# Kernel optimization log

Hardware: AMD Instinct MI355X
Metric: run time of the kernel (lower is better)

## Reference

```python
import jax, jax.numpy as jnp
import numpy as np
from jax import lax

DIM = 180; NH = 6; WH = 16; WW = 16; MH = 8; MW = 8
HD = DIM // (2 * NH)  # 15, head dim; also the (non-sqrt) scale
RMS_EPS = 1.1920929e-07  # torch.finfo(float32).eps (RMSNorm eps=None)

def _conv(x, w, b, pad):
    # x: NHWC, w: HWIO
    return lax.conv_general_dilated(x, w, (1, 1), [(pad, pad), (pad, pad)],
                                    dimension_numbers=('NHWC', 'HWIO', 'NHWC')) + b

def _lrelu(x):
    return jnp.where(x >= 0, x, 0.2 * x)

def _ln(x, w, b, eps=1e-5):
    m = x.mean(-1, keepdims=True)
    v = jnp.mean((x - m) ** 2, -1, keepdims=True)
    return (x - m) / jnp.sqrt(v + eps) * w + b

def _forward(x, dfe_w1, dfe_b1, dfe_w2, dfe_b2, dfe_w3, dfe_b3, dfe_lw, dfe_lb,
             sl_w, sl_b, pos_pw, pos_pb, ln1w, ln1b, l1w, l1b, ln2w, ln2b,
             l2w, l2b, ln3w, ln3b, l3w, l3b, proj_w, proj_b, norm_w):
    B, C, H, W = x.shape
    xh = jnp.transpose(x, (0, 2, 3, 1))  # NHWC
    shortcut = xh
    # DFE: conv branch gated by 1x1 linear branch
    h = _lrelu(_conv(xh, dfe_w1, dfe_b1, 0))
    h = _lrelu(_conv(h, dfe_w2, dfe_b2, 1))
    h = _conv(h, dfe_w3, dfe_b3, 0)
    qv = h * _conv(xh, dfe_lw, dfe_lb, 0)  # (B,H,W,C)
    # window partition
    L = WH * WW
    qv = qv.reshape(B, H // WH, WH, W // WW, WW, C).transpose(0, 1, 3, 2, 4, 5).reshape(-1, L, C)
    Bw = qv.shape[0]
    qv = qv.reshape(Bw, L, 2, NH, HD).transpose(2, 0, 3, 1, 4)
    q, v = qv[0], qv[1]  # (Bw, NH, L, HD)
    # spatial linear projection of v: downsample window -> base window
    rH, rW = WH // MH, WW // MW
    vp = v.reshape(Bw, NH, MH, rH, MW, rW, HD).transpose(0, 1, 2, 4, 6, 3, 5)
    vp = vp.reshape(Bw, NH, MH * MW, HD, rH * rW)
    vp = ((vp @ sl_w) + sl_b)[..., 0]  # (Bw, NH, mapL, HD)
    corr = jnp.einsum('bhlc,bhmc->bhlm', q, vp) / HD  # (Bw, NH, L, mapL)
    # dynamic relative position bias
    bh = jnp.arange(1 - WH, WH, dtype=jnp.float32)
    bw = jnp.arange(1 - WW, WW, dtype=jnp.float32)
    biases = jnp.stack(jnp.meshgrid(bh, bw, indexing='ij')).reshape(2, -1).T  # (nb, 2)
    p = biases @ pos_pw + pos_pb
    p = jax.nn.relu(_ln(p, ln1w, ln1b)) @ l1w + l1b
    p = jax.nn.relu(_ln(p, ln2w, ln2b)) @ l2w + l2b
    pos = jax.nn.relu(_ln(p, ln3w, ln3b)) @ l3w + l3b  # (nb, NH)
    coords = jnp.stack(jnp.meshgrid(jnp.arange(WH), jnp.arange(WW), indexing='ij')).reshape(2, -1)
    rel = coords[:, :, None] - coords[:, None, :]  # (2, L, L)
    idx = (rel[0] + WH - 1) * (2 * WW - 1) + (rel[1] + WW - 1)  # (L, L)
    rpb = pos[idx.reshape(-1)].reshape(L, MH, rH, MW, rW, NH)
    rpb = rpb.transpose(0, 1, 3, 5, 2, 4).reshape(L, MH * MW, NH, rH * rW).mean(-1)
    rpb = rpb.transpose(2, 0, 1)  # (NH, L, mapL)
    corr = corr + rpb[None]
    xs = jnp.einsum('bhlm,bhmc->bhlc', corr, vp).transpose(0, 2, 1, 3).reshape(Bw, L, NH * HD)
    # channel self-correlation
    qc = q.transpose(0, 2, 1, 3).reshape(Bw, L, NH * HD)
    vc = v.transpose(0, 2, 1, 3).reshape(Bw, L, NH * HD)
    cmap = jnp.einsum('blc,bld->bcd', qc, vc) / L  # (Bw, C/2, C/2)
    xc = jnp.einsum('bcd,bld->blc', cmap, vc)  # (Bw, L, C/2)
    # window reverse
    def wrev(win):
        c = win.shape[-1]
        return win.reshape(B, H // WH, W // WW, WH, WW, c).transpose(0, 1, 3, 2, 4, 5).reshape(B, H, W, c)
    xs = wrev(xs.reshape(Bw, WH, WW, NH * HD))
    xc = wrev(xc.reshape(Bw, WH, WW, NH * HD))
    y = jnp.concatenate([xs, xc], -1)  # (B, H, W, C)
    y = y @ proj_w + proj_b
    y = y * (1.0 / jnp.sqrt(jnp.mean(y * y, -1, keepdims=True) + RMS_EPS)) * norm_w
    y = shortcut + y
    return jnp.transpose(y, (0, 3, 1, 2))


def setup_inputs() -> dict:
    key = jax.random.key(0)
    ks = iter(jax.random.split(key, 32))
    def rn(shape, s=0.05):
        return jax.random.normal(next(ks), shape, jnp.float32) * s
    inp = {}
    inp['x'] = jax.random.normal(next(ks), (4, 180, 256, 256), jnp.float32)
    inp['dfe_w1'] = rn((1, 1, 180, 36)); inp['dfe_b1'] = rn((36,))
    inp['dfe_w2'] = rn((3, 3, 36, 36)); inp['dfe_b2'] = rn((36,))
    inp['dfe_w3'] = rn((1, 1, 36, 180)); inp['dfe_b3'] = rn((180,))
    inp['dfe_lw'] = rn((1, 1, 180, 180)); inp['dfe_lb'] = rn((180,))
    inp['sl_w'] = rn((4, 1)); inp['sl_b'] = rn((1,))
    inp['pos_pw'] = rn((2, 11)); inp['pos_pb'] = rn((11,))
    inp['ln1w'] = jnp.ones((11,)); inp['ln1b'] = jnp.zeros((11,))
    inp['l1w'] = rn((11, 11)); inp['l1b'] = rn((11,))
    inp['ln2w'] = jnp.ones((11,)); inp['ln2b'] = jnp.zeros((11,))
    inp['l2w'] = rn((11, 11)); inp['l2b'] = rn((11,))
    inp['ln3w'] = jnp.ones((11,)); inp['ln3b'] = jnp.zeros((11,))
    inp['l3w'] = rn((11, 6)); inp['l3b'] = rn((6,))
    inp['proj_w'] = rn((180, 180)); inp['proj_b'] = rn((180,))
    inp['norm_w'] = jnp.ones((180,))
    return inp


def reference(x, dfe_w1, dfe_b1, dfe_w2, dfe_b2, dfe_w3, dfe_b3, dfe_lw, dfe_lb,
              sl_w, sl_b, pos_pw, pos_pb, ln1w, ln1b, l1w, l1b, ln2w, ln2b,
              l2w, l2b, ln3w, ln3b, l3w, l3b, proj_w, proj_b, norm_w):
    return _forward(x, dfe_w1, dfe_b1, dfe_w2, dfe_b2, dfe_w3, dfe_b3, dfe_lw, dfe_lb,
                    sl_w, sl_b, pos_pw, pos_pb, ln1w, ln1b, l1w, l1b, ln2w, ln2b,
                    l2w, l2b, ln3w, ln3b, l3w, l3b, proj_w, proj_b, norm_w)
```

## Files before the change

### kernel.cpp

```cpp
#include <hip/hip_runtime.h>
#include <stdint.h>

typedef unsigned short u16;
typedef unsigned int   u32;

#define HW 65536

typedef __bf16 bf16x8 __attribute__((ext_vector_type(8)));
typedef float  f32x4  __attribute__((ext_vector_type(4)));

static __device__ __forceinline__ float bf2f(u16 h) {
    u32 u = ((u32)h) << 16;
    return __builtin_bit_cast(float, u);
}
static __device__ __forceinline__ u16 f2bf(float f) {
    u32 u = __builtin_bit_cast(u32, f);
    u += 0x7fffu + ((u >> 16) & 1u);
    return (u16)(u >> 16);
}
static __device__ __forceinline__ void bf2x2(u32 u, float& a, float& b) {
    a = __builtin_bit_cast(float, u << 16);
    b = __builtin_bit_cast(float, u & 0xffff0000u);
}
static __device__ __forceinline__ f32x4 mfma16(bf16x8 a, bf16x8 b, f32x4 c) {
    return __builtin_amdgcn_mfma_f32_16x16x32_bf16(a, b, c, 0, 0, 0);
}

static __device__ __forceinline__ void lnrelu11(float* p, const float* __restrict__ w,
                                                const float* __restrict__ b) {
    float m = 0.f;
    #pragma unroll
    for (int k = 0; k < 11; k++) m += p[k];
    m *= (1.0f / 11.0f);
    float v = 0.f;
    #pragma unroll
    for (int k = 0; k < 11; k++) { float d = p[k] - m; v = fmaf(d, d, v); }
    v *= (1.0f / 11.0f);
    float r = 1.0f / sqrtf(v + 1e-5f);
    #pragma unroll
    for (int k = 0; k < 11; k++) {
        float t = (p[k] - m) * r * w[k] + b[k];
        p[k] = t > 0.f ? t : 0.f;
    }
}

__global__ __launch_bounds__(1024) void k_pos(
    const float* __restrict__ pw, const float* __restrict__ pb,
    const float* __restrict__ ln1w, const float* __restrict__ ln1b,
    const float* __restrict__ l1w, const float* __restrict__ l1b,
    const float* __restrict__ ln2w, const float* __restrict__ ln2b,
    const float* __restrict__ l2w, const float* __restrict__ l2b,
    const float* __restrict__ ln3w, const float* __restrict__ ln3b,
    const float* __restrict__ l3w, const float* __restrict__ l3b,
    float* __restrict__ pos)
{
    int i = threadIdx.x;
    if (i >= 961) return;
    float b0 = (float)(i / 31) - 15.0f;
    float b1 = (float)(i % 31) - 15.0f;
    float p[11], t[11];
    #pragma unroll
    for (int j = 0; j < 11; j++) p[j] = b0 * pw[j] + b1 * pw[11 + j] + pb[j];
    lnrelu11(p, ln1w, ln1b);
    #pragma unroll
    for (int j = 0; j < 11; j++) {
        float s = l1b[j];
        #pragma unroll
        for (int k = 0; k < 11; k++) s = fmaf(p[k], l1w[k * 11 + j], s);
        t[j] = s;
    }
    lnrelu11(t, ln2w, ln2b);
    #pragma unroll
    for (int j = 0; j < 11; j++) {
        float s = l2b[j];
        #pragma unroll
        for (int k = 0; k < 11; k++) s = fmaf(t[k], l2w[k * 11 + j], s);
        p[j] = s;
    }
    lnrelu11(p, ln3w, ln3b);
    #pragma unroll
    for (int h = 0; h < 6; h++) {
        float s = l3b[h];
        #pragma unroll
        for (int k = 0; k < 11; k++) s = fmaf(p[k], l3w[k * 6 + h], s);
        pos[i * 6 + h] = s;
    }
}

__global__ __launch_bounds__(256) void k_rpb(const float* __restrict__ pos,
                                             float* __restrict__ rpb)
{
    int g = blockIdx.x * 256 + threadIdx.x;
    if (g >= 6 * 256 * 64) return;
    int h = g >> 14;
    int l = (g >> 6) & 255;
    int m = g & 63;
    int yl = l >> 4, xl = l & 15;
    int my = m >> 3, mx = m & 7;
    float s = 0.f;
    #pragma unroll
    for (int ry = 0; ry < 2; ry++) {
        #pragma unroll
        for (int rx = 0; rx < 2; rx++) {
            int y2 = my * 2 + ry, x2 = mx * 2 + rx;
            int idx = (yl - y2 + 15) * 31 + (xl - x2 + 15);
            s += pos[idx * 6 + h];
        }
    }
    rpb[g] = 0.25f * s;
}

__global__ __launch_bounds__(256) void k_conv1(const float* __restrict__ x,
                                               const float* __restrict__ w,
                                               const float* __restrict__ b,
                                               u16* __restrict__ h1)
{
    int pix = blockIdx.x * 256 + threadIdx.x;
    int bb = pix >> 16, sp = pix & 65535;
    float acc[36];
    #pragma unroll
    for (int j = 0; j < 36; j++) acc[j] = b[j];
    const float* xp = x + (size_t)bb * 180 * HW + sp;
    for (int c = 0; c < 180; c++) {
        float xv = xp[(size_t)c * HW];
        #pragma unroll
        for (int j = 0; j < 36; j++) acc[j] = fmaf(xv, w[c * 36 + j], acc[j]);
    }
    u16* hp = h1 + (size_t)bb * 36 * HW + sp;
    #pragma unroll
    for (int j = 0; j < 36; j++) {
        float v = acc[j];
        v = v >= 0.f ? v : 0.2f * v;
        hp[(size_t)j * HW] = f2bf(v);
    }
}

__global__ __launch_bounds__(256) void k_conv3(const u16* __restrict__ h1,
                                               const float* __restrict__ w,
                                               const float* __restrict__ b,
                                               u16* __restrict__ h2)
{
    int tx = threadIdx.x, ty = threadIdx.y;
    int x0 = blockIdx.x * 16 + tx;
    int y0 = blockIdx.y * 16 + ty;
    int bb = blockIdx.z;
    float acc[36];
    #pragma unroll
    for (int j = 0; j < 36; j++) acc[j] = b[j];
    const u16* base = h1 + (size_t)bb * 36 * HW;
    for (int ky = 0; ky < 3; ky++) {
        int yy = y0 + ky - 1;
        if (yy < 0 || yy >= 256) continue;
        for (int kx = 0; kx < 3; kx++) {
            int xx = x0 + kx - 1;
            if (xx < 0 || xx >= 256) continue;
            const u16* ip = base + yy * 256 + xx;
            const float* wp = w + ((ky * 3 + kx) * 36) * 36;
            for (int c = 0; c < 36; c++) {
                float v = bf2f(ip[(size_t)c * HW]);
                #pragma unroll
                for (int j = 0; j < 36; j++) acc[j] = fmaf(v, wp[c * 36 + j], acc[j]);
            }
        }
    }
    u16* op = h2 + (size_t)bb * 36 * HW + y0 * 256 + x0;
    #pragma unroll
    for (int j = 0; j < 36; j++) {
        float v = acc[j];
        v = v >= 0.f ? v : 0.2f * v;
        op[(size_t)j * HW] = f2bf(v);
    }
}

__global__ __launch_bounds__(256) void k_wgprep(const float* __restrict__ lw,
                                                const float* __restrict__ w3,
                                                u16* __restrict__ gwh,
                                                u16* __restrict__ gwl,
                                                u16* __restrict__ cwh,
                                                u16* __restrict__ cwl)
{
    int gidx = blockIdx.x * 256 + threadIdx.x;
    if (gidx < 36864) {
        int oc = gidx / 192, k = gidx % 192;
        float v = (oc < 180 && k < 180) ? lw[k * 180 + oc] : 0.f;
        u16 h = f2bf(v);
        float lo = v - bf2f(h);
        gwh[gidx] = h;
        gwl[gidx] = f2bf(lo);
    } else {
        int r = gidx - 36864;
        int oc = r / 64, k = r % 64;
        float v = (oc < 180 && k < 36) ? w3[k * 180 + oc] : 0.f;
        u16 h = f2bf(v);
        float lo = v - bf2f(h);
        cwh[r] = h;
        cwl[r] = f2bf(lo);
    }
}

__global__ __launch_bounds__(256) void k_gate(const u16* __restrict__ h2,
                                              const float* __restrict__ x,
                                              const u16* __restrict__ gwh,
                                              const u16* __restrict__ gwl,
                                              const u16* __restrict__ cwh,
                                              const u16* __restrict__ cwl,
                                              const float* __restrict__ b3,
                                              const float* __restrict__ lb,
                                              u16* __restrict__ qvT)
{
    int t = threadIdx.x;
    int lane = t & 63;
    int g = __builtin_amdgcn_readfirstlane(t >> 6);
    int m = lane & 15, q = lane >> 4;
    int blk = blockIdx.x;
    int w  = blk >> 2;
    int lq = blk & 3;
    int bb = w >> 8, wy = (w >> 4) & 15, wx = w & 15;
    int ocb = g * 48;
    int sp0 = (wy * 16 + lq * 4) * 256 + wx * 16 + m;
    const float* xb = x + (size_t)bb * 180 * HW;
    const u16*  hb = h2 + (size_t)bb * 36 * HW;

    f32x4 accG[3][4], accC[3][4];
    #pragma unroll
    for (int mt = 0; mt < 3; mt++)
        #pragma unroll
        for (int pt = 0; pt < 4; pt++) {
            f32x4 z = {0.f, 0.f, 0.f, 0.f};
            accG[mt][pt] = z;
            accC[mt][pt] = z;
        }

    #pragma unroll 2
    for (int ks = 0; ks < 6; ks++) {
        float xv[4][8];
        #pragma unroll
        for (int pt = 0; pt < 4; pt++)
            #pragma unroll
            for (int j = 0; j < 8; j++) {
                int c = ks * 32 + q * 8 + j;
                if (c > 179) c = 179;
                xv[pt][j] = xb[(size_t)c * HW + sp0 + pt * 256];
            }
        bf16x8 Bh[4], Bl[4];
        #pragma unroll
        for (int pt = 0; pt < 4; pt++)
            #pragma unroll
            for (int j = 0; j < 8; j++) {
                float v = xv[pt][j];
                __bf16 hi = (__bf16)v;
                Bh[pt][j] = hi;
                Bl[pt][j] = (__bf16)(v - (float)hi);
            }
        #pragma unroll
        for (int mt = 0; mt < 3; mt++) {
            bf16x8 Ah = *(const bf16x8*)(gwh + (size_t)(ocb + mt * 16 + m) * 192 + ks * 32 + q * 8);
            bf16x8 Al = *(const bf16x8*)(gwl + (size_t)(ocb + mt * 16 + m) * 192 + ks * 32 + q * 8);
            #pragma unroll
            for (int pt = 0; pt < 4; pt++) {
                accG[mt][pt] = mfma16(Ah, Bh[pt], accG[mt][pt]);
                accG[mt][pt] = mfma16(Al, Bh[pt], accG[mt][pt]);
                accG[mt][pt] = mfma16(Ah, Bl[pt], accG[mt][pt]);
            }
        }
    }

    #pragma unroll
    for (int ks = 0; ks < 2; ks++) {
        bf16x8 B[4];
        #pragma unroll
        for (int pt = 0; pt < 4; pt++)
            #pragma unroll
            for (int j = 0; j < 8; j++) {
                int c = ks * 32 + q * 8 + j;
                if (c > 35) c = 35;
                B[pt][j] = __builtin_bit_cast(__bf16, hb[(size_t)c * HW + sp0 + pt * 256]);
            }
        #pragma unroll
        for (int mt = 0; mt < 3; mt++) {
            bf16x8 Ah = *(const bf16x8*)(cwh + (size_t)(ocb + mt * 16 + m) * 64 + ks * 32 + q * 8);
            bf16x8 Al = *(const bf16x8*)(cwl + (size_t)(ocb + mt * 16 + m) * 64 + ks * 32 + q * 8);
            #pragma unroll
            for (int pt = 0; pt < 4; pt++) {
                accC[mt][pt] = mfma16(Ah, B[pt], accC[mt][pt]);
                accC[mt][pt] = mfma16(Al, B[pt], accC[mt][pt]);
            }
        }
    }

    u16* qw = qvT + (size_t)w * 180 * 256 + lq * 64 + m;
    #pragma unroll
    for (int mt = 0; mt < 3; mt++)
        #pragma unroll
        for (int r = 0; r < 4; r++) {
            int oc = ocb + mt * 16 + q * 4 + r;
            if (oc < 180) {
                float bc = b3[oc], bg = lb[oc];
                #pragma unroll
                for (int pt = 0; pt < 4; pt++) {
                    float ah = accC[mt][pt][r] + bc;
                    float al = accG[mt][pt][r] + bg;
                    qw[(size_t)oc * 256 + pt * 16] = f2bf(ah * al);
                }
            }
        }
}

__global__ __launch_bounds__(256) void k_spat(const u16* __restrict__ qvT,
                                              const float* __restrict__ rpb,
                                              const float* __restrict__ slw,
                                              const float* __restrict__ slb,
                                              u16* __restrict__ yp)
{
    __shared__ __align__(16) float vp[6144];
    int w = blockIdx.x;
    int bb = w >> 8, wy = (w >> 4) & 15, wx = w & 15;
    int t = threadIdx.x;
    int lane = t & 63, wv = t >> 6;
    const u16* qw = qvT + (size_t)w * 180 * 256;
    float s0 = slw[0], s1 = slw[1], s2 = slw[2], s3 = slw[3], sb = slb[0];
    for (int o = t; o < 384; o += 256) vp[(o >> 6) * 1024 + (o & 63) * 16 + 15] = 0.f;
    for (int it = 0; it < 23; it++) {
        int p = wv + it * 4;
        if (p < 90) {
            int mm = lane;
            int l0 = (mm >> 3) * 32 + (mm & 7) * 2;
            const u16* rp2 = qw + (size_t)(90 + p) * 256;
            float s = sb + s0 * bf2f(rp2[l0]) + s1 * bf2f(rp2[l0 + 1])
                         + s2 * bf2f(rp2[l0 + 16]) + s3 * bf2f(rp2[l0 + 17]);
            vp[(p / 15) * 1024 + mm * 16 + (p % 15)] = s;
        }
    }
    __syncthreads();
    int l = t;
    size_t pixl = (size_t)((bb * 256 + wy * 16 + (l >> 4)) * 256 + wx * 16 + (l & 15));
    u16* op = yp + pixl * 192;
    ((u32*)op)[45] = 0u; ((u32*)op)[46] = 0u; ((u32*)op)[47] = 0u;
    for (int h = 0; h < 6; h++) {
        float q[16];
        #pragma unroll
        for (int d = 0; d < 15; d++) q[d] = bf2f(qw[(size_t)(h * 15 + d) * 256 + l]);
        q[15] = 0.f;
        float acc[16];
        #pragma unroll
        for (int d = 0; d < 16; d++) acc[d] = 0.f;
        const float* rp = rpb + ((h * 256 + l) << 6);
        const float4* vph = (const float4*)(vp + (h << 10));
        for (int m0 = 0; m0 < 64; m0 += 4) {
            float ra[4];
            *(float4*)ra = *(const float4*)(rp + m0);
            #pragma unroll
            for (int mm = 0; mm < 4; mm++) {
                int m = m0 + mm;
                float wvv[16];
                ((float4*)wvv)[0] = vph[m * 4 + 0];
                ((float4*)wvv)[1] = vph[m * 4 + 1];
                ((float4*)wvv)[2] = vph[m * 4 + 2];
                ((float4*)wvv)[3] = vph[m * 4 + 3];
                float s = 0.f;
                #pragma unroll
                for (int d2 = 0; d2 < 16; d2++) s = fmaf(q[d2], wvv[d2], s);
                s = s * (1.0f / 15.0f) + ra[mm];
                #pragma unroll
                for (int d2 = 0; d2 < 16; d2++) acc[d2] = fmaf(s, wvv[d2], acc[d2]);
            }
        }
        #pragma unroll
        for (int d = 0; d < 15; d++) op[h * 15 + d] = f2bf(acc[d]);
    }
}

__global__ __launch_bounds__(256) void k_chan(const u16* __restrict__ qvT,
                                              u16* __restrict__ yp)
{
    __shared__ __align__(16) u16 cm[96 * 104];
    __shared__ __align__(16) u16 xcb[128 * 104];
    int w = blockIdx.x;
    int bb = w >> 8, wy = (w >> 4) & 15, wx = w & 15;
    int t = threadIdx.x;
    int lane = t & 63, wv = t >> 6;
    int m = lane & 15, quad = lane >> 4;
    const u16* qw = qvT + (size_t)w * 180 * 256;

    int ct0 = (wv & 1) * 3, dt0 = (wv >> 1) * 3;
    f32x4 acc[3][3];
    #pragma unroll
    for (int i = 0; i < 3; i++)
        #pragma unroll
        for (int j = 0; j < 3; j++) {
            f32x4 z = {0.f, 0.f, 0.f, 0.f};
            acc[i][j] = z;
        }
    #pragma unroll
    for (int ks = 0; ks < 8; ks++) {
        bf16x8 A[3], B[3];
        #pragma unroll
        for (int i = 0; i < 3; i++)
            A[i] = *(const bf16x8*)(qw + (size_t)((ct0 + i) * 16 + m) * 256 + ks * 32 + quad * 8);
        #pragma unroll
        for (int j = 0; j < 3; j++) {
            int d = (dt0 + j) * 16 + m;
            int dd = d > 89 ? 89 : d;
            B[j] = *(const bf16x8*)(qw + (size_t)(90 + dd) * 256 + ks * 32 + quad * 8);
        }
        #pragma unroll
        for (int i = 0; i < 3; i++)
            #pragma unroll
            for (int j = 0; j < 3; j++)
                acc[i][j] = mfma16(A[i], B[j], acc[i][j]);
    }
    #pragma unroll
    for (int i = 0; i < 3; i++)
        #pragma unroll
        for (int j = 0; j < 3; j++)
            #pragma unroll
            for (int r = 0; r < 4; r++)
                cm[((ct0 + i) * 16 + quad * 4 + r) * 104 + (dt0 + j) * 16 + m] =
                    f2bf(acc[i][j][r] * (1.0f / 256.0f));
    __syncthreads();
    if (t < 96) {
        u32* z = (u32*)(cm + t * 104 + 90);
        z[0] = 0; z[1] = 0; z[2] = 0;
    }
    __syncthreads();

    int base_pix = (bb * 256 + wy * 16) * 256 + wx * 16;
    const __bf16* qwb = (const __bf16*)qw;
    for (int half = 0; half < 2; half++) {
        #pragma unroll
        for (int i = 0; i < 2; i++) {
            int ltl = wv * 2 + i;
            int lt = half * 8 + ltl;
            bf16x8 A[3];
            #pragma unroll
            for (int ks = 0; ks < 3; ks++) {
                const __bf16* colp = qwb + lt * 16 + m;
                #pragma unroll
                for (int j2 = 0; j2 < 8; j2++) {
                    int d = ks * 32 + quad * 8 + j2;
                    int dd = d > 89 ? 89 : d;
                    A[ks][j2] = colp[(size_t)(90 + dd) * 256];
                }
            }
            for (int ct = 0; ct < 6; ct++) {
                f32x4 c4 = {0.f, 0.f, 0.f, 0.f};
                #pragma unroll
                for (int ks = 0; ks < 3; ks++) {
                    bf16x8 B = *(const bf16x8*)(cm + (ct * 16 + m) * 104 + ks * 32 + quad * 8);
                    c4 = mfma16(A[ks], B, c4);
                }
                #pragma unroll
                for (int r = 0; r < 4; r++)
                    xcb[(ltl * 16 + quad * 4 + r) * 104 + ct * 16 + m] = f2bf(c4[r]);
            }
        }
        __syncthreads();
        #pragma unroll
        for (int it = 0; it < 6; it++) {
            int gg = t + it * 256;
            int lrow = gg / 12, seg = gg % 12;
            int l = half * 128 + lrow;
            int pix = base_pix + (l >> 4) * 256 + (l & 15);
            *(uint4*)(yp + (size_t)pix * 192 + 96 + seg * 8) =
                *(const uint4*)(xcb + lrow * 104 + seg * 8);
        }
        __syncthreads();
    }
}

__global__ __launch_bounds__(256) void k_wprep(const float* __restrict__ pjw,
                                               u16* __restrict__ whiT,
                                               u16* __restrict__ wloT)
{
    int g = blockIdx.x * 256 + threadIdx.x;
    int oc = g / 192, k = g % 192;
    int kp = -1;
    if (k < 90) kp = k;
    else if (k >= 96 && k < 186) kp = k - 6;
    float v = (kp >= 0 && oc < 180) ? pjw[kp * 180 + oc] : 0.f;
    u16 h = f2bf(v);
    float lo = v - bf2f(h);
    whiT[g] = h;
    wloT[g] = f2bf(lo);
}

__global__ __launch_bounds__(256) void k_proj(const u16* __restrict__ yp,
                                              const float* __restrict__ x,
                                              const u16* __restrict__ whiT,
                                              const u16* __restrict__ wloT,
                                              const float* __restrict__ pb,
                                              const float* __restrict__ nw,
                                              float* __restrict__ out)
{
    __shared__ float part[4][4][16];
    int t = threadIdx.x;
    int lane = t & 63;
    int g = __builtin_amdgcn_readfirstlane(t >> 6);
    int m = lane & 15, q = lane >> 4;
    int pix0 = blockIdx.x * 64;
    int ocbase = g * 48;

    f32x4 acc[3][4];
    #pragma unroll
    for (int mt = 0; mt < 3; mt++)
        #pragma unroll
        for (int pt = 0; pt < 4; pt++) {
            f32x4 z = {0.f, 0.f, 0.f, 0.f};
            acc[mt][pt] = z;
        }

    const u16* bbase = yp + (size_t)pix0 * 192;
    #pragma unroll 2
    for (int ks = 0; ks < 6; ks++) {
        bf16x8 B[4];
        #pragma unroll
        for (int pt = 0; pt < 4; pt++)
            B[pt] = *(const bf16x8*)(bbase + (size_t)(pt * 16 + m) * 192 + ks * 32 + q * 8);
        #pragma unroll
        for (int mt = 0; mt < 3; mt++) {
            bf16x8 Ah = *(const bf16x8*)(whiT + (size_t)(ocbase + mt * 16 + m) * 192 + ks * 32 + q * 8);
            bf16x8 Al = *(const bf16x8*)(wloT + (size_t)(ocbase + mt * 16 + m) * 192 + ks * 32 + q * 8);
            #pragma unroll
            for (int pt = 0; pt < 4; pt++) {
                acc[mt][pt] = mfma16(Ah, B[pt], acc[mt][pt]);
                acc[mt][pt] = mfma16(Al, B[pt], acc[mt][pt]);
            }
        }
    }

    float pbv[3][4], nwv[3][4];
    #pragma unroll
    for (int mt = 0; mt < 3; mt++)
        #pragma unroll
        for (int r = 0; r < 4; r++) {
            int oc = ocbase + mt * 16 + q * 4 + r;
            bool ok = oc < 180;
            pbv[mt][r] = ok ? pb[oc] : 0.f;
            nwv[mt][r] = ok ? nw[oc] : 0.f;
        }
    float ss[4] = {0.f, 0.f, 0.f, 0.f};
    #pragma unroll
    for (int mt = 0; mt < 3; mt++)
        #pragma unroll
        for (int pt = 0; pt < 4; pt++)
            #pragma unroll
            for (int r = 0; r < 4; r++) {
                float y = acc[mt][pt][r] + pbv[mt][r];
                acc[mt][pt][r] = y;
                ss[pt] = fmaf(y, y, ss[pt]);
            }
    #pragma unroll
    for (int pt = 0; pt < 4; pt++) {
        ss[pt] += __shfl_xor(ss[pt], 16);
        ss[pt] += __shfl_xor(ss[pt], 32);
    }
    if (q == 0) {
        #pragma unroll
        for (int pt = 0; pt < 4; pt++) part[g][pt][m] = ss[pt];
    }
    __syncthreads();
    float scale[4];
    #pragma unroll
    for (int pt = 0; pt < 4; pt++) {
        float tot = part[0][pt][m] + part[1][pt][m] + part[2][pt][m] + part[3][pt][m];
        scale[pt] = 1.0f / sqrtf(tot * (1.0f / 180.0f) + 1.1920929e-7f);
    }

    int bb = pix0 >> 16, sp0 = pix0 & 65535;
    const float* xb = x + (size_t)bb * 180 * HW + sp0 + m;
    float* ob = out + (size_t)bb * 180 * HW + sp0 + m;
    #pragma unroll
    for (int mt = 0; mt < 3; mt++)
        #pragma unroll
        for (int r = 0; r < 4; r++) {
            int oc = ocbase + mt * 16 + q * 4 + r;
            if (oc < 180) {
                #pragma unroll
                for (int pt = 0; pt < 4; pt++) {
                    size_t off = (size_t)oc * HW + pt * 16;
                    ob[off] = xb[off] + acc[mt][pt][r] * scale[pt] * nwv[mt][r];
                }
            }
        }
}

extern "C" void kernel_launch(void* const* d_in, const int* in_sizes, int n_in,
                              void* d_out, int out_size, void* d_ws, size_t ws_size,
                              hipStream_t stream)
{
    const float* x    = (const float*)d_in[0];
    const float* w1   = (const float*)d_in[1];
    const float* b1   = (const float*)d_in[2];
    const float* w2   = (const float*)d_in[3];
    const float* b2   = (const float*)d_in[4];
    const float* w3   = (const float*)d_in[5];
    const float* b3   = (const float*)d_in[6];
    const float* lw   = (const float*)d_in[7];
    const float* lb   = (const float*)d_in[8];
    const float* slw  = (const float*)d_in[9];
    const float* slb  = (const float*)d_in[10];
    const float* pw   = (const float*)d_in[11];
    const float* pb   = (const float*)d_in[12];
    const float* ln1w = (const float*)d_in[13];
    const float* ln1b = (const float*)d_in[14];
    const float* l1w  = (const float*)d_in[15];
    const float* l1b  = (const float*)d_in[16];
    const float* ln2w = (const float*)d_in[17];
    const float* ln2b = (const float*)d_in[18];
    const float* l2w  = (const float*)d_in[19];
    const float* l2b  = (const float*)d_in[20];
    const float* ln3w = (const float*)d_in[21];
    const float* ln3b = (const float*)d_in[22];
    const float* l3w  = (const float*)d_in[23];
    const float* l3b  = (const float*)d_in[24];
    const float* pjw  = (const float*)d_in[25];
    const float* pjb  = (const float*)d_in[26];
    const float* nw   = (const float*)d_in[27];
    float* out = (float*)d_out;

    char* ws = (char*)d_ws;
    float* pos = (float*)(ws + 0);
    float* rpb = (float*)(ws + 24576);
    u16*  h2  = (u16*)(ws + 417792);
    u16*  whiT = (u16*)(ws + 417792);
    u16*  wloT = (u16*)(ws + 417792 + 73728);
    u16*  h1  = (u16*)(ws + 19292160);
    u16*  qvT = (u16*)(ws + 19292160);
    u16*  yp  = (u16*)(ws + 113664000);
    u16*  gwh = (u16*)(ws + 113664000);
    u16*  gwl = (u16*)(ws + 113664000 + 73728);
    u16*  cwh = (u16*)(ws + 113664000 + 147456);
    u16*  cwl = (u16*)(ws + 113664000 + 172032);

    k_wgprep<<<dim3(192), dim3(256), 0, stream>>>(lw, w3, gwh, gwl, cwh, cwl);
    k_pos<<<dim3(1), dim3(1024), 0, stream>>>(pw, pb, ln1w, ln1b, l1w, l1b,
                                              ln2w, ln2b, l2w, l2b, ln3w, ln3b,
                                              l3w, l3b, pos);
    k_rpb<<<dim3(384), dim3(256), 0, stream>>>(pos, rpb);
    k_conv1<<<dim3(1024), dim3(256), 0, stream>>>(x, w1, b1, h1);
    k_conv3<<<dim3(16, 16, 4), dim3(16, 16), 0, stream>>>(h1, w2, b2, h2);
    k_gate<<<dim3(4096), dim3(256), 0, stream>>>(h2, x, gwh, gwl, cwh, cwl,
                                                 b3, lb, qvT);
    k_wprep<<<dim3(144), dim3(256), 0, stream>>>(pjw, whiT, wloT);
    k_spat<<<dim3(1024), dim3(256), 0, stream>>>(qvT, rpb, slw, slb, yp);
    k_chan<<<dim3(1024), dim3(256), 0, stream>>>(qvT, yp);
    k_proj<<<dim3(4096), dim3(256), 0, stream>>>(yp, x, whiT, wloT, pjb, nw, out);
}
```

Baseline: 1.089 ms.

## Stage gate inputs in LDS and vectorize projection epilogue via shared transpose

In the gate kernel, the 180 input channels and 36 hidden channels for each 64-pixel tile are loaded once into swizzled shared memory, using global_load_lds for x. The MFMA operands are then built from LDS instead of scattered per-element global loads. In the projection kernel, the scaled accumulators are written through a shared staging buffer in two phases, so the residual read and output store become 16-byte vector accesses along pixels. This adds LDS usage and barriers, which may reduce occupancy.

```diff
diff --git a/kernel.cpp b/kernel.cpp
--- a/kernel.cpp
+++ b/kernel.cpp
@@ -208,6 +208,8 @@
                                               const float* __restrict__ lb,
                                               u16* __restrict__ qvT)
 {
+    __shared__ __align__(16) float xs[180 * 64];
+    __shared__ __align__(16) u16  hs[36 * 64];
     int t = threadIdx.x;
     int lane = t & 63;
     int g = __builtin_amdgcn_readfirstlane(t >> 6);
@@ -217,9 +219,32 @@
     int lq = blk & 3;
     int bb = w >> 8, wy = (w >> 4) & 15, wx = w & 15;
     int ocb = g * 48;
-    int sp0 = (wy * 16 + lq * 4) * 256 + wx * 16 + m;
+    int y0 = wy * 16 + lq * 4;
+    int xc0 = wx * 16;
     const float* xb = x + (size_t)bb * 180 * HW;
     const u16*  hb = h2 + (size_t)bb * 36 * HW;
+
+    for (int s = g; s < 45; s += 4) {
+        int c = s * 4 + (lane >> 4);
+        int swz = (c >> 3) & 1;
+        int pp = (lane & 15) ^ (swz << 2);
+        int p0 = pp * 4;
+        int prow = p0 >> 4, pcol = p0 & 15;
+        const float* gp = xb + (size_t)c * HW + (y0 + prow) * 256 + xc0 + pcol;
+        __builtin_amdgcn_global_load_lds(
+            (const __attribute__((address_space(1))) void*)gp,
+            (__attribute__((address_space(3))) void*)(xs + s * 256),
+            16, 0, 0);
+    }
+    for (int idx = t; idx < 288; idx += 256) {
+        int c = idx >> 3, j = idx & 7;
+        int p0 = j * 8;
+        int prow = p0 >> 4, pcol = p0 & 15;
+        uint4 v = *(const uint4*)(hb + (size_t)c * HW + (y0 + prow) * 256 + xc0 + pcol);
+        int swz = (c >> 3) & 1;
+        *(uint4*)(hs + c * 64 + (p0 ^ (swz << 4))) = v;
+    }
+    __syncthreads();
 
     f32x4 accG[3][4], accC[3][4];
     #pragma unroll
@@ -233,21 +258,15 @@
 
     #pragma unroll 2
     for (int ks = 0; ks < 6; ks++) {
-        float xv[4][8];
+        bf16x8 Bh[4], Bl[4];
         #pragma unroll
         for (int pt = 0; pt < 4; pt++)
             #pragma unroll
             for (int j = 0; j < 8; j++) {
                 int c = ks * 32 + q * 8 + j;
                 if (c > 179) c = 179;
-                xv[pt][j] = xb[(size_t)c * HW + sp0 + pt * 256];
-            }
-        bf16x8 Bh[4], Bl[4];
-        #pragma unroll
-        for (int pt = 0; pt < 4; pt++)
-            #pragma unroll
-            for (int j = 0; j < 8; j++) {
-                float v = xv[pt][j];
+                int p = pt * 16 + m;
+                float v = xs[c * 64 + (p ^ (((c >> 3) & 1) << 4))];
                 __bf16 hi = (__bf16)v;
                 Bh[pt][j] = hi;
                 Bl[pt][j] = (__bf16)(v - (float)hi);
@@ -274,7 +293,8 @@
             for (int j = 0; j < 8; j++) {
                 int c = ks * 32 + q * 8 + j;
                 if (c > 35) c = 35;
-                B[pt][j] = __builtin_bit_cast(__bf16, hb[(size_t)c * HW + sp0 + pt * 256]);
+                int p = pt * 16 + m;
+                B[pt][j] = __builtin_bit_cast(__bf16, hs[c * 64 + (p ^ (((c >> 3) & 1) << 4))]);
             }
         #pragma unroll
         for (int mt = 0; mt < 3; mt++) {
@@ -476,7 +496,7 @@
     int oc = g / 192, k = g % 192;
     int kp = -1;
     if (k < 90) kp = k;
-    else if (k >= 96 && k < 186) kp = k - 6;
+    else if (k >= 96 && k <= 185) kp = k - 6;
     float v = (kp >= 0 && oc < 180) ? pjw[kp * 180 + oc] : 0.f;
     u16 h = f2bf(v);
     float lo = v - bf2f(h);
@@ -492,6 +512,7 @@
                                               const float* __restrict__ nw,
                                               float* __restrict__ out)
 {
+    __shared__ __align__(16) float st[96 * 68];
     __shared__ float part[4][4][16];
     int t = threadIdx.x;
     int lane = t & 63;
@@ -565,23 +586,43 @@
         float tot = part[0][pt][m] + part[1][pt][m] + part[2][pt][m] + part[3][pt][m];
         scale[pt] = 1.0f / sqrtf(tot * (1.0f / 180.0f) + 1.1920929e-7f);
     }
+    #pragma unroll
+    for (int mt = 0; mt < 3; mt++)
+        #pragma unroll
+        for (int pt = 0; pt < 4; pt++)
+            #pragma unroll
+            for (int r = 0; r < 4; r++)
+                acc[mt][pt][r] = acc[mt][pt][r] * scale[pt] * nwv[mt][r];
 
     int bb = pix0 >> 16, sp0 = pix0 & 65535;
-    const float* xb = x + (size_t)bb * 180 * HW + sp0 + m;
-    float* ob = out + (size_t)bb * 180 * HW + sp0 + m;
-    #pragma unroll
-    for (int mt = 0; mt < 3; mt++)
-        #pragma unroll
-        for (int r = 0; r < 4; r++) {
-            int oc = ocbase + mt * 16 + q * 4 + r;
-            if (oc < 180) {
-                #pragma unroll
-                for (int pt = 0; pt < 4; pt++) {
-                    size_t off = (size_t)oc * HW + pt * 16;
-                    ob[off] = xb[off] + acc[mt][pt][r] * scale[pt] * nwv[mt][r];
+    const float* xb = x + (size_t)bb * 180 * HW + sp0;
+    float* ob = out + (size_t)bb * 180 * HW + sp0;
+    #pragma unroll
+    for (int ph = 0; ph < 2; ph++) {
+        if ((g >> 1) == ph) {
+            int rb = (g & 1) * 48;
+            #pragma unroll
+            for (int mt = 0; mt < 3; mt++)
+                #pragma unroll
+                for (int r = 0; r < 4; r++) {
+                    int row = rb + mt * 16 + q * 4 + r;
+                    #pragma unroll
+                    for (int pt = 0; pt < 4; pt++)
+                        st[row * 68 + pt * 16 + m] = acc[mt][pt][r];
                 }
-            }
-        }
+        }
+        __syncthreads();
+        int nch = ph ? 1344 : 1536;
+        for (int i = t; i < nch; i += 256) {
+            int row = i >> 4, j = i & 15;
+            int oc = ph * 96 + row;
+            f32x4 d = *(const f32x4*)(st + row * 68 + j * 4);
+            size_t off = (size_t)oc * HW + j * 4;
+            f32x4 xv = *(const f32x4*)(xb + off);
+            *(f32x4*)(ob + off) = d + xv;
+        }
+        __syncthreads();
+    }
 }
 
 extern "C" void kernel_launch(void* const* d_in, const int* in_sizes, int n_in,
```

Result: faster. 1.048 ms (-3.7%).
